# Optimization experiments

Hardware: AMD Instinct MI355X
Metric: run time of the kernel (lower is better)

## Reference

```python
import jax, jax.numpy as jnp
import numpy as np

B, ORDER, S, D, H = 64, 2, 256, 256, 8
HD = D // H  # head_dim = 32


def setup_inputs() -> dict:
    key = jax.random.key(0)
    ks = jax.random.split(key, 6)
    stdv = 1.0 / np.sqrt(HD)
    return {
        "x": jax.random.normal(ks[0], (B, ORDER, S, D), jnp.float32),
        "A": jax.random.randint(ks[1], (B, ORDER, S, S), 0, 5, jnp.int32),
        # params stacked as [order, conv(1|2), ...]
        "Wp": jax.random.normal(ks[2], (ORDER, 2, D, D), jnp.float32) * stdv,
        "bp": jnp.zeros((ORDER, 2, D), jnp.float32),
        "att_src": jax.random.normal(ks[3], (ORDER, 2, H, HD), jnp.float32) * stdv,
        "att_dst": jax.random.normal(ks[4], (ORDER, 2, H, HD), jnp.float32) * stdv,
        "gbias": jnp.zeros((ORDER, 2, D), jnp.float32),
        "prelu_a": 0.25 * jnp.ones((D,), jnp.float32),
    }


def _gat(x, edge, W, b, a_src, a_dst, gb):
    """Dense additive GAT over a [B,S,S] boolean adjacency. Eval mode (dropout inert)."""
    Bt, St, Dt = x.shape
    x = x @ W + b                                   # project (bias=True)
    xh = x.reshape(Bt, St, H, HD)
    a_s = jnp.einsum('bshd,hd->bsh', xh, a_src)     # per-source score
    a_d = jnp.einsum('bthd,hd->bth', xh, a_dst)     # per-dest score
    alpha = a_s[:, :, None, :] + a_d[:, None, :, :]  # [B, S_src, S_dst, H]
    alpha = jnp.where(edge[..., None], alpha, 0.0)   # masked_fill((A != 1), 0)
    alpha = jnp.where(alpha >= 0, alpha, 0.2 * alpha)  # leaky_relu(0.2)
    alpha = jax.nn.softmax(alpha, axis=1)            # stable softmax over source axis
    out = jnp.einsum('bsth,bshd->bthd', alpha, xh).reshape(Bt, St, Dt)
    return out + x + gb                              # add_self_loops + bias


def reference(x, A, Wp, bp, att_src, att_dst, gbias, prelu_a):
    # A1 = (A==2)+(A==4); A2 = (A==3)+(A==4); edge iff value == 1
    A1 = (A == 2) | (A == 4)
    A2 = (A == 3) | (A == 4)
    hs = []
    for i in range(ORDER):  # order is a small structural constant (=2)
        h1 = _gat(x[:, i], A1[:, i], Wp[i, 0], bp[i, 0], att_src[i, 0], att_dst[i, 0], gbias[i, 0])
        h2 = _gat(x[:, i], A2[:, i], Wp[i, 1], bp[i, 1], att_src[i, 1], att_dst[i, 1], gbias[i, 1])
        hs.append(h1 + h2)
    h = jnp.stack(hs, axis=1)                       # [B, order, S, D]
    out = h + h.mean(axis=1, keepdims=True)
    out = jnp.where(out >= 0, out, prelu_a * out)   # PReLU(dim)
    return out
```

## Files before the change

### kernel.cpp

```cpp
#include <hip/hip_runtime.h>
#include <hip/hip_bf16.h>
#include <math.h>

typedef __bf16 bf16;
typedef __bf16 bf16x4 __attribute__((ext_vector_type(4)));
typedef __bf16 bf16x8 __attribute__((ext_vector_type(8)));
typedef float f32x4 __attribute__((ext_vector_type(4)));
typedef unsigned int u32;

#define LOG2E 1.44269504f

__device__ inline float fast_exp2(float x) {
#if __has_builtin(__builtin_amdgcn_exp2f)
    return __builtin_amdgcn_exp2f(x);
#else
    return exp2f(x);
#endif
}

#define GL2LDS(gp, lp) __builtin_amdgcn_global_load_lds( \
    (const __attribute__((address_space(1))) u32*)(gp),  \
    (__attribute__((address_space(3))) u32*)(lp), 16, 0, 0)


__global__ void prep_k(const float* __restrict__ x, const float* __restrict__ Wp,
                       const int* __restrict__ A, bf16* __restrict__ xb,
                       bf16* __restrict__ Wt, unsigned* __restrict__ m1,
                       unsigned* __restrict__ m2) {
    int bid = blockIdx.x;
    int tid = threadIdx.x;
    if (bid < 4096) {
        int gid = bid * 256 + tid;
        const f32x4* xp = (const f32x4*)x + (size_t)gid * 2;
        f32x4 a = xp[0], b4 = xp[1];
        bf16x8 o;
#pragma unroll
        for (int c = 0; c < 4; ++c) { o[c] = (bf16)a[c]; o[c + 4] = (bf16)b4[c]; }
        ((bf16x8*)xb)[gid] = o;
    } else if (bid < 5120) {
        int gid = (bid - 4096) * 256 + tid;
        int k = gid & 255;
        int n = (gid >> 8) & 255;
        int ij = gid >> 16;
        Wt[gid] = (bf16)Wp[(ij * 256 + k) * 256 + n];
    } else {
        int pb = bid - 5120;
        int sh = pb & 1;
        int ijb = pb >> 1;
        const int* Ab = A + ((size_t)ijb << 16);
        unsigned w1 = 0, w2 = 0;
#pragma unroll 8
        for (int sl = 0; sl < 128; ++sl) {
            int s = sh * 128 + sl;
            int av = Ab[s * 256 + tid];
            unsigned f1 = (av == 2 || av == 4) ? 1u : 0u;
            unsigned f2 = (av == 3 || av == 4) ? 1u : 0u;
            w1 |= f1 << (s & 31);
            w2 |= f2 << (s & 31);
            if ((s & 31) == 31) {
                int kc = s >> 5;
                m1[(ijb * 8 + kc) * 256 + tid] = w1;
                m2[(ijb * 8 + kc) * 256 + tid] = w2;
                w1 = 0; w2 = 0;
            }
        }
    }
}

__launch_bounds__(256)
__global__ void proj_gemm(const bf16* __restrict__ xb, const bf16* __restrict__ Wt,
                          const float* __restrict__ bp, const float* __restrict__ att_src,
                          const float* __restrict__ att_dst, bf16* __restrict__ Vt,
                          float* __restrict__ asb, float* __restrict__ adb) {
    __shared__ char smem[35840 + 1024];
    bf16* As = (bf16*)smem;
    bf16* Bs = (bf16*)(smem + 8192);
    bf16* TL = (bf16*)smem;
    float* attL = (float*)(smem + 35840);

    int tid = threadIdx.x;
    int mt = blockIdx.x, nt = blockIdx.y, i = blockIdx.z;
    int n0 = nt * 128;
    int j = n0 >> 8, d0 = n0 & 255;
    int ij = i * 2 + j;
    int m0 = mt * 128;
    int b = m0 >> 8, shalf = (m0 >> 7) & 1;

    {
        int which = tid >> 7, rest = tid & 127;
        const float* ap = which ? att_dst : att_src;
        attL[tid] = ap[(ij * 8 + (d0 >> 5) + (rest >> 5)) * 32 + (rest & 31)];
    }

    int c0 = tid, c1 = tid + 256;
    int r0 = c0 >> 2, k80 = (c0 & 3) * 8;
    int r1 = c1 >> 2, k81 = (c1 & 3) * 8;
    const bf16* ga0 = xb + (((size_t)((b * 2 + i) * 256 + shalf * 128 + r0)) << 8) + k80;
    const bf16* ga1 = xb + (((size_t)((b * 2 + i) * 256 + shalf * 128 + r1)) << 8) + k81;
    const bf16* gb0 = Wt + (((size_t)(ij * 256 + d0 + r0)) << 8) + k80;
    const bf16* gb1 = Wt + (((size_t)(ij * 256 + d0 + r1)) << 8) + k81;
    bf16* la0 = As + c0 * 8;
    bf16* la1 = As + c1 * 8;
    bf16* lb0 = Bs + c0 * 8;
    bf16* lb1 = Bs + c1 * 8;

    int wave = tid >> 6, lane = tid & 63;
    int wd = (wave & 1) * 64, ws = (wave >> 1) * 64;
    int lrow = lane & 15, quad = lane >> 4;

    f32x4 acc[4][4];
#pragma unroll
    for (int a = 0; a < 4; ++a)
#pragma unroll
        for (int c = 0; c < 4; ++c) acc[a][c] = (f32x4){0.f, 0.f, 0.f, 0.f};

    for (int kc = 0; kc < 8; ++kc) {
        int k0 = kc * 32;
        GL2LDS(ga0 + k0, la0);
        GL2LDS(ga1 + k0, la1);
        GL2LDS(gb0 + k0, lb0);
        GL2LDS(gb1 + k0, lb1);
        __syncthreads();
        bf16x8 wf[4], xf[4];
#pragma unroll
        for (int dj = 0; dj < 4; ++dj)
            wf[dj] = *(const bf16x8*)&Bs[(wd + dj * 16 + lrow) * 32 + quad * 8];
#pragma unroll
        for (int sj = 0; sj < 4; ++sj)
            xf[sj] = *(const bf16x8*)&As[(ws + sj * 16 + lrow) * 32 + quad * 8];
#pragma unroll
        for (int dj = 0; dj < 4; ++dj)
#pragma unroll
            for (int sj = 0; sj < 4; ++sj)
                acc[dj][sj] = __builtin_amdgcn_mfma_f32_16x16x32_bf16(wf[dj], xf[sj], acc[dj][sj], 0, 0, 0);
        __syncthreads();
    }

#pragma unroll
    for (int dj = 0; dj < 4; ++dj) {
#pragma unroll
        for (int r = 0; r < 4; ++r) {
            int dl = wd + dj * 16 + quad * 4 + r;
            float bias = bp[ij * 256 + d0 + dl];
#pragma unroll
            for (int sj = 0; sj < 4; ++sj)
                TL[dl * 140 + ws + sj * 16 + lrow] = (bf16)(acc[dj][sj][r] + bias);
        }
    }
    __syncthreads();

    {
        int dl = tid >> 1, sh64 = (tid & 1) * 64;
        const bf16* src = TL + dl * 140 + sh64;
        bf16* dst = Vt + (((size_t)(ij * 64 + b)) << 16) + (size_t)(d0 + dl) * 256
                    + shalf * 128 + sh64;
#pragma unroll
        for (int q = 0; q < 16; ++q)
            *(bf16x4*)(dst + q * 4) = *(const bf16x4*)(src + q * 4);
    }

    {
        int s = tid & 127, which = tid >> 7;
        const float* av = attL + which * 128;
        float* outp = which ? adb : asb;
#pragma unroll
        for (int hl = 0; hl < 4; ++hl) {
            float accs = 0.f;
#pragma unroll
            for (int d = 0; d < 32; ++d)
                accs += (float)TL[(hl * 32 + d) * 140 + s] * av[hl * 32 + d];
            int hg = (d0 >> 5) + hl;
            outp[((ij * 64 + b) * 8 + hg) * 256 + shalf * 128 + s] = accs * LOG2E;
        }
    }
}

__launch_bounds__(256, 2)
__global__ void attn_k(const bf16* __restrict__ Vt, const unsigned* __restrict__ m1,
                       const unsigned* __restrict__ m2, const float* __restrict__ asb,
                       const float* __restrict__ adb, const float* __restrict__ gbias,
                       const float* __restrict__ prelu_a, float* __restrict__ out) {
    int bid = blockIdx.x;
    int tt = bid & 3, hg = (bid >> 2) & 1, b = bid >> 3;
    int t0 = tt * 64;
    int tid = threadIdx.x, wave = tid >> 6, lane = tid & 63;
    int lrow = lane & 15, quad = lane >> 4;
    int h = hg * 4 + wave;

    __shared__ float    as_l[2][2][4][256];
    __shared__ unsigned ml[2][2][8][64];
    __shared__ float    l_lds[2][2][4][64];

#pragma unroll
    for (int p = 0; p < 16; ++p) {
        int idx = p * 256 + tid;
        int i = idx >> 11, c = (idx >> 10) & 1, w = (idx >> 8) & 3, s = idx & 255;
        as_l[i][c][w][s] = asb[(((i * 2 + c) * 64 + b) * 8 + hg * 4 + w) * 256 + s];
    }
#pragma unroll
    for (int p = 0; p < 8; ++p) {
        int idx = p * 256 + tid;
        int i = idx >> 10, c = (idx >> 9) & 1, kc = (idx >> 6) & 7, tl = idx & 63;
        ml[i][c][kc][tl] = (c ? m2 : m1)[((b * 2 + i) * 8 + kc) * 256 + t0 + tl];
    }
    float ad_r[2][2][4];
#pragma unroll
    for (int i = 0; i < 2; ++i)
#pragma unroll
        for (int c = 0; c < 2; ++c)
#pragma unroll
            for (int mi = 0; mi < 4; ++mi)
                ad_r[i][c][mi] = adb[(((i * 2 + c) * 64 + b) * 8 + h) * 256 + t0 + mi * 16 + lrow];
    __syncthreads();

    const bf16* vtp[2][2];
#pragma unroll
    for (int i = 0; i < 2; ++i)
#pragma unroll
        for (int c = 0; c < 2; ++c)
            vtp[i][c] = Vt + (((size_t)(((i * 2 + c) * 64 + b) * 8 + h)) << 13);

    f32x4 acc[2][2][4][2];
#pragma unroll
    for (int i = 0; i < 2; ++i)
#pragma unroll
        for (int c = 0; c < 2; ++c)
#pragma unroll
            for (int mi = 0; mi < 4; ++mi)
#pragma unroll
                for (int ni = 0; ni < 2; ++ni) acc[i][c][mi][ni] = (f32x4){0.f, 0.f, 0.f, 0.f};
    float lsum[2][2][4];
#pragma unroll
    for (int i = 0; i < 2; ++i)
#pragma unroll
        for (int c = 0; c < 2; ++c)
#pragma unroll
            for (int mi = 0; mi < 4; ++mi) lsum[i][c][mi] = 0.f;

    for (int kc = 0; kc < 8; ++kc) {
        int s0 = kc * 32;
        bf16x8 bfr[2][2][2];
#pragma unroll
        for (int i = 0; i < 2; ++i)
#pragma unroll
            for (int c = 0; c < 2; ++c)
#pragma unroll
                for (int ni = 0; ni < 2; ++ni)
                    bfr[i][c][ni] = *(const bf16x8*)(vtp[i][c] + (size_t)(ni * 16 + lrow) * 256 + s0 + quad * 8);
#pragma unroll
        for (int i = 0; i < 2; ++i) {
#pragma unroll
            for (int c = 0; c < 2; ++c) {
                f32x4 asv0 = *(const f32x4*)&as_l[i][c][wave][s0 + quad * 8];
                f32x4 asv1 = *(const f32x4*)&as_l[i][c][wave][s0 + quad * 8 + 4];
#pragma unroll
                for (int mi = 0; mi < 4; ++mi) {
                    unsigned wb = ml[i][c][kc][mi * 16 + lrow] >> (quad * 8);
                    float ad = ad_r[i][c][mi];
                    bf16x8 af;
#pragma unroll
                    for (int j = 0; j < 8; ++j) {
                        float u = (j < 4 ? asv0[j] : asv1[j - 4]) + ad;
                        u = fmaxf(u, 0.2f * u);
                        u = ((wb >> j) & 1u) ? u : 0.f;
                        float e = fast_exp2(u);
                        lsum[i][c][mi] += e;
                        af[j] = (bf16)e;
                    }
                    acc[i][c][mi][0] = __builtin_amdgcn_mfma_f32_16x16x32_bf16(af, bfr[i][c][0], acc[i][c][mi][0], 0, 0, 0);
                    acc[i][c][mi][1] = __builtin_amdgcn_mfma_f32_16x16x32_bf16(af, bfr[i][c][1], acc[i][c][mi][1], 0, 0, 0);
                }
            }
        }
    }

#pragma unroll
    for (int i = 0; i < 2; ++i)
#pragma unroll
        for (int c = 0; c < 2; ++c)
#pragma unroll
            for (int mi = 0; mi < 4; ++mi) {
                float l = lsum[i][c][mi];
                l += __shfl_xor(l, 16, 64);
                l += __shfl_xor(l, 32, 64);
                if (lane < 16) l_lds[i][c][wave][mi * 16 + lane] = l;
            }
    __syncthreads();

#pragma unroll
    for (int ni = 0; ni < 2; ++ni) {
        int dcol = h * 32 + ni * 16 + lrow;
        float gb0 = gbias[0 * 256 + dcol] + gbias[1 * 256 + dcol];
        float gb1 = gbias[2 * 256 + dcol] + gbias[3 * 256 + dcol];
        float pa = prelu_a[dcol];
        const bf16* r00 = vtp[0][0] + (size_t)(ni * 16 + lrow) * 256 + t0;
        const bf16* r01 = vtp[0][1] + (size_t)(ni * 16 + lrow) * 256 + t0;
        const bf16* r10 = vtp[1][0] + (size_t)(ni * 16 + lrow) * 256 + t0;
        const bf16* r11 = vtp[1][1] + (size_t)(ni * 16 + lrow) * 256 + t0;
#pragma unroll
        for (int mi = 0; mi < 4; ++mi) {
            bf16x4 rv00 = *(const bf16x4*)(r00 + mi * 16 + quad * 4);
            bf16x4 rv01 = *(const bf16x4*)(r01 + mi * 16 + quad * 4);
            bf16x4 rv10 = *(const bf16x4*)(r10 + mi * 16 + quad * 4);
            bf16x4 rv11 = *(const bf16x4*)(r11 + mi * 16 + quad * 4);
#pragma unroll
            for (int r = 0; r < 4; ++r) {
                int tl = mi * 16 + quad * 4 + r;
                int t = t0 + tl;
                float v0 = acc[0][0][mi][ni][r] * __builtin_amdgcn_rcpf(l_lds[0][0][wave][tl])
                         + acc[0][1][mi][ni][r] * __builtin_amdgcn_rcpf(l_lds[0][1][wave][tl])
                         + (float)rv00[r] + (float)rv01[r] + gb0;
                float v1 = acc[1][0][mi][ni][r] * __builtin_amdgcn_rcpf(l_lds[1][0][wave][tl])
                         + acc[1][1][mi][ni][r] * __builtin_amdgcn_rcpf(l_lds[1][1][wave][tl])
                         + (float)rv10[r] + (float)rv11[r] + gb1;
                float mn = 0.5f * (v0 + v1);
                float a0 = v0 + mn, a1 = v1 + mn;
                a0 = a0 >= 0.f ? a0 : pa * a0;
                a1 = a1 >= 0.f ? a1 : pa * a1;
                out[(((size_t)((b * 2 + 0) * 256 + t)) << 8) + dcol] = a0;
                out[(((size_t)((b * 2 + 1) * 256 + t)) << 8) + dcol] = a1;
            }
        }
    }
}

extern "C" void kernel_launch(void* const* d_in, const int* in_sizes, int n_in,
                              void* d_out, int out_size, void* d_ws, size_t ws_size,
                              hipStream_t stream) {
    const float* x       = (const float*)d_in[0];
    const int*   A       = (const int*)d_in[1];
    const float* Wp      = (const float*)d_in[2];
    const float* bp      = (const float*)d_in[3];
    const float* att_src = (const float*)d_in[4];
    const float* att_dst = (const float*)d_in[5];
    const float* gbias   = (const float*)d_in[6];
    const float* prelu_a = (const float*)d_in[7];
    float* out = (float*)d_out;

    char* ws = (char*)d_ws;
    bf16*     Wt  = (bf16*)ws;
    unsigned* m1  = (unsigned*)(ws + 524288);
    unsigned* m2  = (unsigned*)(ws + 1572864);
    float*    asb = (float*)(ws + 2621440);
    float*    adb = (float*)(ws + 4718592);
    bf16*     xb  = (bf16*)(ws + 6815744);
    bf16*     Vt  = (bf16*)(ws + 23592960);

    prep_k<<<5376, 256, 0, stream>>>(x, Wp, A, xb, Wt, m1, m2);
    dim3 gproj(128, 4, 2);
    proj_gemm<<<gproj, 256, 0, stream>>>(xb, Wt, bp, att_src, att_dst, Vt, asb, adb);
    attn_k<<<512, 256, 0, stream>>>(Vt, m1, m2, asb, adb, gbias, prelu_a, out);
}
```

Baseline: 212.0 us.

## Fuse attention-score dot products into GEMM epilogue and halve attention dest tile

In the projection GEMM, the per-source and per-destination attention scores are now accumulated from the fp32 accumulators in registers and reduced with cross-lane shuffles. This replaces the separate pass that re-read the bf16 transposed tile from LDS. The attention kernel now handles 32 destination rows per block instead of 64, doubling the grid to 1024 blocks and raising the launch-bounds occupancy hint to 3. This gives more parallelism and less register pressure, at the cost of reloading the per-block source scores and V tiles twice as often.

```diff
diff --git a/kernel.cpp b/kernel.cpp
--- a/kernel.cpp
+++ b/kernel.cpp
@@ -136,15 +136,56 @@
         __syncthreads();
     }
 
+    float sc[2][2][4];
+#pragma unroll
+    for (int w2 = 0; w2 < 2; ++w2)
+#pragma unroll
+        for (int hf = 0; hf < 2; ++hf)
+#pragma unroll
+            for (int sj = 0; sj < 4; ++sj) sc[w2][hf][sj] = 0.f;
 #pragma unroll
     for (int dj = 0; dj < 4; ++dj) {
+        int hf = dj >> 1;
 #pragma unroll
         for (int r = 0; r < 4; ++r) {
             int dl = wd + dj * 16 + quad * 4 + r;
             float bias = bp[ij * 256 + d0 + dl];
-#pragma unroll
-            for (int sj = 0; sj < 4; ++sj)
-                TL[dl * 140 + ws + sj * 16 + lrow] = (bf16)(acc[dj][sj][r] + bias);
+            float avs = attL[dl];
+            float avd = attL[128 + dl];
+#pragma unroll
+            for (int sj = 0; sj < 4; ++sj) {
+                float v = acc[dj][sj][r] + bias;
+                TL[dl * 140 + ws + sj * 16 + lrow] = (bf16)v;
+                sc[0][hf][sj] += v * avs;
+                sc[1][hf][sj] += v * avd;
+            }
+        }
+    }
+#pragma unroll
+    for (int w2 = 0; w2 < 2; ++w2)
+#pragma unroll
+        for (int hf = 0; hf < 2; ++hf)
+#pragma unroll
+            for (int sj = 0; sj < 4; ++sj) {
+                float v = sc[w2][hf][sj];
+                v += __shfl_xor(v, 16, 64);
+                v += __shfl_xor(v, 32, 64);
+                sc[w2][hf][sj] = v;
+            }
+    if (lane < 16) {
+        int hbase = (d0 >> 5) + (wd >> 5);
+#pragma unroll
+        for (int w2 = 0; w2 < 2; ++w2) {
+            float* outp = w2 ? adb : asb;
+#pragma unroll
+            for (int hf = 0; hf < 2; ++hf) {
+                int hh = hbase + hf;
+#pragma unroll
+                for (int sj = 0; sj < 4; ++sj) {
+                    int s = ws + sj * 16 + lane;
+                    outp[((ij * 64 + b) * 8 + hh) * 256 + shalf * 128 + s] = sc[w2][hf][sj] * LOG2E;
+                }
+            }
         }
     }
     __syncthreads();
@@ -158,38 +199,23 @@
         for (int q = 0; q < 16; ++q)
             *(bf16x4*)(dst + q * 4) = *(const bf16x4*)(src + q * 4);
     }
-
-    {
-        int s = tid & 127, which = tid >> 7;
-        const float* av = attL + which * 128;
-        float* outp = which ? adb : asb;
-#pragma unroll
-        for (int hl = 0; hl < 4; ++hl) {
-            float accs = 0.f;
-#pragma unroll
-            for (int d = 0; d < 32; ++d)
-                accs += (float)TL[(hl * 32 + d) * 140 + s] * av[hl * 32 + d];
-            int hg = (d0 >> 5) + hl;
-            outp[((ij * 64 + b) * 8 + hg) * 256 + shalf * 128 + s] = accs * LOG2E;
-        }
-    }
-}
-
-__launch_bounds__(256, 2)
+}
+
+__launch_bounds__(256, 3)
 __global__ void attn_k(const bf16* __restrict__ Vt, const unsigned* __restrict__ m1,
                        const unsigned* __restrict__ m2, const float* __restrict__ asb,
                        const float* __restrict__ adb, const float* __restrict__ gbias,
                        const float* __restrict__ prelu_a, float* __restrict__ out) {
     int bid = blockIdx.x;
-    int tt = bid & 3, hg = (bid >> 2) & 1, b = bid >> 3;
-    int t0 = tt * 64;
+    int tt = bid & 7, hg = (bid >> 3) & 1, b = bid >> 4;
+    int t0 = tt * 32;
     int tid = threadIdx.x, wave = tid >> 6, lane = tid & 63;
     int lrow = lane & 15, quad = lane >> 4;
     int h = hg * 4 + wave;
 
     __shared__ float    as_l[2][2][4][256];
-    __shared__ unsigned ml[2][2][8][64];
-    __shared__ float    l_lds[2][2][4][64];
+    __shared__ unsigned ml[2][2][8][32];
+    __shared__ float    l_lds[2][2][4][32];
 
 #pragma unroll
     for (int p = 0; p < 16; ++p) {
@@ -198,18 +224,18 @@
         as_l[i][c][w][s] = asb[(((i * 2 + c) * 64 + b) * 8 + hg * 4 + w) * 256 + s];
     }
 #pragma unroll
-    for (int p = 0; p < 8; ++p) {
+    for (int p = 0; p < 4; ++p) {
         int idx = p * 256 + tid;
-        int i = idx >> 10, c = (idx >> 9) & 1, kc = (idx >> 6) & 7, tl = idx & 63;
+        int i = idx >> 9, c = (idx >> 8) & 1, kc = (idx >> 5) & 7, tl = idx & 31;
         ml[i][c][kc][tl] = (c ? m2 : m1)[((b * 2 + i) * 8 + kc) * 256 + t0 + tl];
     }
-    float ad_r[2][2][4];
-#pragma unroll
-    for (int i = 0; i < 2; ++i)
-#pragma unroll
-        for (int c = 0; c < 2; ++c)
-#pragma unroll
-            for (int mi = 0; mi < 4; ++mi)
+    float ad_r[2][2][2];
+#pragma unroll
+    for (int i = 0; i < 2; ++i)
+#pragma unroll
+        for (int c = 0; c < 2; ++c)
+#pragma unroll
+            for (int mi = 0; mi < 2; ++mi)
                 ad_r[i][c][mi] = adb[(((i * 2 + c) * 64 + b) * 8 + h) * 256 + t0 + mi * 16 + lrow];
     __syncthreads();
 
@@ -220,22 +246,22 @@
         for (int c = 0; c < 2; ++c)
             vtp[i][c] = Vt + (((size_t)(((i * 2 + c) * 64 + b) * 8 + h)) << 13);
 
-    f32x4 acc[2][2][4][2];
-#pragma unroll
-    for (int i = 0; i < 2; ++i)
-#pragma unroll
-        for (int c = 0; c < 2; ++c)
-#pragma unroll
-            for (int mi = 0; mi < 4; ++mi)
+    f32x4 acc[2][2][2][2];
+#pragma unroll
+    for (int i = 0; i < 2; ++i)
+#pragma unroll
+        for (int c = 0; c < 2; ++c)
+#pragma unroll
+            for (int mi = 0; mi < 2; ++mi)
 #pragma unroll
                 for (int ni = 0; ni < 2; ++ni) acc[i][c][mi][ni] = (f32x4){0.f, 0.f, 0.f, 0.f};
-    float lsum[2][2][4];
-#pragma unroll
-    for (int i = 0; i < 2; ++i)
-#pragma unroll
-        for (int c = 0; c < 2; ++c)
-#pragma unroll
-            for (int mi = 0; mi < 4; ++mi) lsum[i][c][mi] = 0.f;
+    float lsum[2][2][2];
+#pragma unroll
+    for (int i = 0; i < 2; ++i)
+#pragma unroll
+        for (int c = 0; c < 2; ++c)
+#pragma unroll
+            for (int mi = 0; mi < 2; ++mi) lsum[i][c][mi] = 0.f;
 
     for (int kc = 0; kc < 8; ++kc) {
         int s0 = kc * 32;
@@ -254,7 +280,7 @@
                 f32x4 asv0 = *(const f32x4*)&as_l[i][c][wave][s0 + quad * 8];
                 f32x4 asv1 = *(const f32x4*)&as_l[i][c][wave][s0 + quad * 8 + 4];
 #pragma unroll
-                for (int mi = 0; mi < 4; ++mi) {
+                for (int mi = 0; mi < 2; ++mi) {
                     unsigned wb = ml[i][c][kc][mi * 16 + lrow] >> (quad * 8);
                     float ad = ad_r[i][c][mi];
                     bf16x8 af;
@@ -279,7 +305,7 @@
 #pragma unroll
         for (int c = 0; c < 2; ++c)
 #pragma unroll
-            for (int mi = 0; mi < 4; ++mi) {
+            for (int mi = 0; mi < 2; ++mi) {
                 float l = lsum[i][c][mi];
                 l += __shfl_xor(l, 16, 64);
                 l += __shfl_xor(l, 32, 64);
@@ -298,7 +324,7 @@
         const bf16* r10 = vtp[1][0] + (size_t)(ni * 16 + lrow) * 256 + t0;
         const bf16* r11 = vtp[1][1] + (size_t)(ni * 16 + lrow) * 256 + t0;
 #pragma unroll
-        for (int mi = 0; mi < 4; ++mi) {
+        for (int mi = 0; mi < 2; ++mi) {
             bf16x4 rv00 = *(const bf16x4*)(r00 + mi * 16 + quad * 4);
             bf16x4 rv01 = *(const bf16x4*)(r01 + mi * 16 + quad * 4);
             bf16x4 rv10 = *(const bf16x4*)(r10 + mi * 16 + quad * 4);
@@ -349,5 +375,5 @@
     prep_k<<<5376, 256, 0, stream>>>(x, Wp, A, xb, Wt, m1, m2);
     dim3 gproj(128, 4, 2);
     proj_gemm<<<gproj, 256, 0, stream>>>(xb, Wt, bp, att_src, att_dst, Vt, asb, adb);
-    attn_k<<<512, 256, 0, stream>>>(Vt, m1, m2, asb, adb, gbias, prelu_a, out);
-}
+    attn_k<<<1024, 256, 0, stream>>>(Vt, m1, m2, asb, adb, gbias, prelu_a, out);
+}
```

Result: slower. 231.8 us (+9.3%).
